# Performance work log

Measured on AMD Instinct MI355X. Metric: run time of the kernel, lower is better.

Reference implementation:

```python
import jax, jax.numpy as jnp
import numpy as np

NUM_ITERATIONS = 5
EPSILON_0 = 1.0
EPS = 1e-20


def setup_inputs() -> dict:
    key = jax.random.key(0)
    k1, k2 = jax.random.split(key)
    B, NIN, NOUT = 8192, 3072, 512
    x = jax.random.uniform(k1, (B, NIN), dtype=jnp.float32)
    w = jax.random.uniform(k2, (NOUT, NIN), dtype=jnp.float32)
    # weights setter normalizes rows to sum to 1
    w = w / w.sum(axis=1, keepdims=True)
    h_initial = jnp.full((NOUT,), 1.0 / NOUT, dtype=jnp.float32)
    return {"x": x, "weights": w, "h_initial": h_initial}


def reference(x, weights, h_initial):
    # x: [B, NIN], weights: [NOUT, NIN], h_initial: [NOUT]
    x = x / (x.sum(axis=1, keepdims=True) + EPS)  # input normalization in forward()
    B = x.shape[0]
    h = jnp.broadcast_to(h_initial[None, :], (B, h_initial.shape[0]))

    def step(h, _):
        # Original: h_w = h[:,:,None]*W[None]; h_w /= h_w.sum(1,keepdim)+eps;
        #           h_w = (h_w * x[:,None,:]).sum(-1)
        # Equivalent without materializing [B, NOUT, NIN]:
        denom = h @ weights                       # [B, NIN] = sum_n h_bn W_nk
        h_w = h * ((x / (denom + EPS)) @ weights.T)  # [B, NOUT]
        h_new = h + EPSILON_0 * h_w               # epsilon_0 > 0 branch
        h_new = h_new / (h_new.sum(axis=1, keepdims=True) + EPS)
        return h_new, None

    h, _ = jax.lax.scan(step, h, None, length=NUM_ITERATIONS)
    return h
```

## Files before the change

### kernel.cpp

```cpp
#include <hip/hip_runtime.h>


#define NIN 3072
#define NOUT 512

using f32x4 = __attribute__((ext_vector_type(4))) float;
using i32x8 = __attribute__((ext_vector_type(8))) int;

union frag32 { i32x8 v; uint4 q[2]; };

#define MFMA128(A, B, C) \
    __builtin_amdgcn_mfma_scale_f32_16x16x128_f8f6f4( \
        (A), (B), (C), 0, 0, 0, (int)0x7f7f7f7f, 0, (int)0x7f7f7f7f)

__device__ __forceinline__ unsigned short f2bf(float f) {
    unsigned int u = __builtin_bit_cast(unsigned int, f);
    return (unsigned short)((u + 0x7fffu + ((u >> 16) & 1u)) >> 16);
}
__device__ __forceinline__ float bf2f(unsigned short s) {
    unsigned int u = ((unsigned int)s) << 16;
    return __builtin_bit_cast(float, u);
}

#define LDS_BARRIER() do {                                   \
    asm volatile("s_waitcnt lgkmcnt(0)" ::: "memory");       \
    __builtin_amdgcn_s_barrier();                            \
    asm volatile("" ::: "memory");                           \
} while (0)

__global__ void prep_all(const float* __restrict__ x,
                         const float* __restrict__ W,
                         const float* __restrict__ h_init,
                         unsigned short* __restrict__ X2,
                         unsigned char* __restrict__ W1,
                         unsigned char* __restrict__ W2,
                         float* __restrict__ d0inv) {
    __shared__ float wsum[4];
    __shared__ float dred[8][32];
    const int bb = blockIdx.x;
    const int t  = threadIdx.x;

    if (bb < 8192) {
        const int b = bb;
        const float4* r4 = reinterpret_cast<const float4*>(x + (size_t)b * NIN);
        float s = 0.f;
        float4 v0 = r4[t], v1 = r4[t + 256], v2 = r4[t + 512];
        s = v0.x + v0.y + v0.z + v0.w + v1.x + v1.y + v1.z + v1.w + v2.x + v2.y + v2.z + v2.w;
        #pragma unroll
        for (int off = 32; off > 0; off >>= 1) s += __shfl_down(s, off, 64);
        int w = t >> 6, l = t & 63;
        if (l == 0) wsum[w] = s;
        __syncthreads();
        float inv = 1.0f / (wsum[0] + wsum[1] + wsum[2] + wsum[3] + 1e-20f);
        unsigned short* orow = X2 + (size_t)b * NIN;
        #pragma unroll
        for (int c = 0; c < 3; ++c) {
            float4 v = (c == 0) ? v0 : (c == 1) ? v1 : v2;
            ushort4 o;
            o.x = f2bf(v.x * inv); o.y = f2bf(v.y * inv);
            o.z = f2bf(v.z * inv); o.w = f2bf(v.w * inv);
            *reinterpret_cast<ushort4*>(orow + (t + c * 256) * 4) = o;
        }
    } else if (bb < 8192 + 384) {
        int tt = (bb - 8192) * 256 + t;
        unsigned int words[8];
        if (tt < 49152) {
            int l = tt & 63, g = tt >> 6;
            int s = g >> 5, rem = g & 31, w = rem >> 2, nt = rem & 3;
            int n = w * 64 + nt * 16 + (l & 15);
            int kbase = s * 128 + ((l >> 4) << 5);
            const float* src = W + (size_t)n * NIN + kbase;
            #pragma unroll
            for (int q = 0; q < 8; ++q) {
                float v0 = src[q * 4 + 0] * 4096.0f, v1 = src[q * 4 + 1] * 4096.0f;
                float v2 = src[q * 4 + 2] * 4096.0f, v3 = src[q * 4 + 3] * 4096.0f;
                int pk = __builtin_amdgcn_cvt_pk_fp8_f32(v0, v1, 0, false);
                pk     = __builtin_amdgcn_cvt_pk_fp8_f32(v2, v3, pk, true);
                words[q] = (unsigned int)pk;
            }
            uint4* dst = reinterpret_cast<uint4*>(W2 + (size_t)tt * 32);
            dst[0] = *reinterpret_cast<uint4*>(&words[0]);
            dst[1] = *reinterpret_cast<uint4*>(&words[4]);
        } else {
            int u = tt - 49152;
            int l = u & 63, g = u >> 6;
            int c = g & 3, sw = g >> 2;
            int w = sw & 7, s = sw >> 3;
            int kout = s * 128 + w * 16 + (l & 15);
            int nbase = c * 128 + ((l >> 4) << 5);
            #pragma unroll
            for (int q = 0; q < 8; ++q) {
                float v0 = W[(size_t)(nbase + q * 4 + 0) * NIN + kout] * 4096.0f;
                float v1 = W[(size_t)(nbase + q * 4 + 1) * NIN + kout] * 4096.0f;
                float v2 = W[(size_t)(nbase + q * 4 + 2) * NIN + kout] * 4096.0f;
                float v3 = W[(size_t)(nbase + q * 4 + 3) * NIN + kout] * 4096.0f;
                int pk = __builtin_amdgcn_cvt_pk_fp8_f32(v0, v1, 0, false);
                pk     = __builtin_amdgcn_cvt_pk_fp8_f32(v2, v3, pk, true);
                words[q] = (unsigned int)pk;
            }
            uint4* dst = reinterpret_cast<uint4*>(W1 + (size_t)u * 32);
            dst[0] = *reinterpret_cast<uint4*>(&words[0]);
            dst[1] = *reinterpret_cast<uint4*>(&words[4]);
        }
    } else {
        int kb = bb - 8576;
        int kid = t & 31, nsub = t >> 5;
        int k = kb * 32 + kid;
        int n0 = nsub * 64;
        float s = 0.f;
        const float* p = W + (size_t)n0 * NIN + k;
        #pragma unroll 8
        for (int n = 0; n < 64; ++n) s += h_init[n0 + n] * p[(size_t)n * NIN];
        dred[nsub][kid] = s;
        __syncthreads();
        if (t < 32) {
            float sm = 1e-20f;
            #pragma unroll
            for (int j = 0; j < 8; ++j) sm += dred[j][t];
            d0inv[kb * 32 + t] = 1.0f / sm;
        }
    }
}

__global__ __launch_bounds__(512, 1) void nnmf_main(
    const unsigned short* __restrict__ X2,
    const unsigned char* __restrict__ W1,
    const unsigned char* __restrict__ W2,
    const float* __restrict__ d0inv,
    const float* __restrict__ h_init,
    float* __restrict__ out)
{
    __shared__ unsigned char  h8_lds[32 * 528];
    __shared__ unsigned short x_lds[32 * 136];
    __shared__ unsigned char  r8_lds[32 * 144];
    __shared__ float red[8][32];

    const int tid = threadIdx.x;
    const int w  = tid >> 6;
    const int l  = tid & 63;
    const int lo = l & 15;
    const int hi = l >> 4;
    const int b0 = blockIdx.x * 32;

    float h_reg[2][4][4];
    #pragma unroll
    for (int nt = 0; nt < 4; ++nt) {
        float hv = h_init[w * 64 + nt * 16 + lo];
        #pragma unroll
        for (int m = 0; m < 2; ++m)
            #pragma unroll
            for (int i = 0; i < 4; ++i)
                h_reg[m][nt][i] = hv;
    }

    const int xrow = tid >> 4, xcc = tid & 15;
    const uint4* xg = reinterpret_cast<const uint4*>(X2 + (size_t)(b0 + xrow) * NIN + xcc * 8);
    unsigned short* xdst = &x_lds[xrow * 136 + xcc * 8];

    const unsigned char* w1base = W1 + (size_t)w * 8192 + (size_t)l * 32;
    const unsigned char* w2base = W2 + ((size_t)(w * 4) * 64 + l) * 32;

    *reinterpret_cast<uint4*>(xdst) = xg[0];
    uint4 xnext = xg[16];
    frag32 w1buf[4];
    __syncthreads();

    const float DSCL = 9.5367431640625e-07f;
    const float TS   = 1.0f / 65536.0f;
    f32x4 tacc[2][4];

    for (int it = 0; it < 5; ++it) {
        #pragma unroll
        for (int m = 0; m < 2; ++m)
            #pragma unroll
            for (int nt = 0; nt < 4; ++nt)
                tacc[m][nt] = (f32x4){0.f, 0.f, 0.f, 0.f};

        for (int s = 0; s < 24; ++s) {
            const int sn  = (s + 1 == 24) ? 0 : s + 1;
            const int sn2 = (s + 2 >= 24) ? (s + 2 - 24) : s + 2;

            uint4 xfut = xg[sn2 * 16];

            frag32 w2v[4];
            {
                const unsigned char* w2p = w2base + (size_t)s * 65536;
                #pragma unroll
                for (int nt = 0; nt < 4; ++nt) {
                    const uint4* p = reinterpret_cast<const uint4*>(w2p + nt * 2048);
                    w2v[nt].q[0] = p[0];
                    w2v[nt].q[1] = p[1];
                }
            }

            f32x4 d0, d1;
            float dv = 0.f;
            if (it == 0) {
                dv = d0inv[s * 128 + w * 16 + lo];
            } else {
                f32x4 a0 = {0,0,0,0}, a1 = {0,0,0,0};
                #pragma unroll
                for (int c = 0; c < 4; ++c) {
                    frag32 ha0, ha1;
                    const uint4* p0 = reinterpret_cast<const uint4*>(
                        &h8_lds[lo * 528 + c * 128 + hi * 32]);
                    const uint4* p1 = reinterpret_cast<const uint4*>(
                        &h8_lds[(16 + lo) * 528 + c * 128 + hi * 32]);
                    ha0.q[0] = p0[0]; ha0.q[1] = p0[1];
                    ha1.q[0] = p1[0]; ha1.q[1] = p1[1];
                    a0 = MFMA128(ha0.v, w1buf[c].v, a0);
                    a1 = MFMA128(ha1.v, w1buf[c].v, a1);
                }
                d0 = a0;
                d1 = a1;
            }

            #pragma unroll
            for (int i = 0; i < 4; ++i) {
                int row0 = hi * 4 + i;
                float x0 = bf2f(x_lds[row0 * 136 + w * 16 + lo]) * 16.0f;
                float x1 = bf2f(x_lds[(16 + row0) * 136 + w * 16 + lo]) * 16.0f;
                float r0, r1;
                if (it == 0) { r0 = x0 * dv; r1 = x1 * dv; }
                else {
                    r0 = x0 * __builtin_amdgcn_rcpf(fmaf(d0[i], DSCL, 1e-20f));
                    r1 = x1 * __builtin_amdgcn_rcpf(fmaf(d1[i], DSCL, 1e-20f));
                }
                int c0 = __builtin_amdgcn_cvt_pk_fp8_f32(r0, r0, 0, false);
                int c1 = __builtin_amdgcn_cvt_pk_fp8_f32(r1, r1, 0, false);
                r8_lds[row0 * 144 + w * 16 + lo] = (unsigned char)(c0 & 0xff);
                r8_lds[(16 + row0) * 144 + w * 16 + lo] = (unsigned char)(c1 & 0xff);
            }
            LDS_BARRIER();

            {
                frag32 ra;
                const uint4* p = reinterpret_cast<const uint4*>(&r8_lds[lo * 144 + hi * 32]);
                ra.q[0] = p[0]; ra.q[1] = p[1];
                #pragma unroll
                for (int nt = 0; nt < 4; ++nt)
                    tacc[0][nt] = MFMA128(ra.v, w2v[nt].v, tacc[0][nt]);
            }

            if (it > 0 || s == 23) {
                const unsigned char* w1p = w1base + (size_t)sn * 65536;
                #pragma unroll
                for (int c = 0; c < 4; ++c) {
                    const uint4* p = reinterpret_cast<const uint4*>(w1p + c * 2048);
                    w1buf[c].q[0] = p[0];
                    w1buf[c].q[1] = p[1];
                }
            }

            {
                frag32 ra;
                const uint4* p = reinterpret_cast<const uint4*>(&r8_lds[(16 + lo) * 144 + hi * 32]);
                ra.q[0] = p[0]; ra.q[1] = p[1];
                #pragma unroll
                for (int nt = 0; nt < 4; ++nt)
                    tacc[1][nt] = MFMA128(ra.v, w2v[nt].v, tacc[1][nt]);
            }

            *reinterpret_cast<uint4*>(xdst) = xnext;
            xnext = xfut;
            LDS_BARRIER();
        }

        float p[2][4];
        #pragma unroll
        for (int m = 0; m < 2; ++m)
            #pragma unroll
            for (int i = 0; i < 4; ++i) p[m][i] = 0.f;

        #pragma unroll
        for (int m = 0; m < 2; ++m)
            #pragma unroll
            for (int nt = 0; nt < 4; ++nt)
                #pragma unroll
                for (int i = 0; i < 4; ++i) {
                    float v = h_reg[m][nt][i] * (1.f + tacc[m][nt][i] * TS);
                    h_reg[m][nt][i] = v;
                    p[m][i] += v;
                }
        #pragma unroll
        for (int mask = 1; mask < 16; mask <<= 1)
            #pragma unroll
            for (int m = 0; m < 2; ++m)
                #pragma unroll
                for (int i = 0; i < 4; ++i)
                    p[m][i] += __shfl_xor(p[m][i], mask, 64);
        if (lo == 0) {
            #pragma unroll
            for (int m = 0; m < 2; ++m)
                #pragma unroll
                for (int i = 0; i < 4; ++i)
                    red[w][m * 16 + hi * 4 + i] = p[m][i];
        }
        __syncthreads();
        float inv[2][4];
        #pragma unroll
        for (int m = 0; m < 2; ++m)
            #pragma unroll
            for (int i = 0; i < 4; ++i) {
                int row = m * 16 + hi * 4 + i;
                float S = 0.f;
                #pragma unroll
                for (int ww = 0; ww < 8; ++ww) S += red[ww][row];
                inv[m][i] = 1.f / (S + 1e-20f);
            }

        if (it < 4) {
            #pragma unroll
            for (int m = 0; m < 2; ++m)
                #pragma unroll
                for (int nt = 0; nt < 4; ++nt)
                    #pragma unroll
                    for (int i = 0; i < 4; ++i) {
                        int row = m * 16 + hi * 4 + i;
                        int col = w * 64 + nt * 16 + lo;
                        float hv = h_reg[m][nt][i] * inv[m][i];
                        h_reg[m][nt][i] = hv;
                        int c = __builtin_amdgcn_cvt_pk_fp8_f32(hv * 256.0f, hv * 256.0f, 0, false);
                        h8_lds[row * 528 + col] = (unsigned char)(c & 0xff);
                    }
            __syncthreads();
        } else {
            #pragma unroll
            for (int m = 0; m < 2; ++m)
                #pragma unroll
                for (int nt = 0; nt < 4; ++nt)
                    #pragma unroll
                    for (int i = 0; i < 4; ++i) {
                        int row = m * 16 + hi * 4 + i;
                        int col = w * 64 + nt * 16 + lo;
                        out[(size_t)(b0 + row) * 512 + col] = h_reg[m][nt][i] * inv[m][i];
                    }
        }
    }
}

extern "C" void kernel_launch(void* const* d_in, const int* in_sizes, int n_in,
                              void* d_out, int out_size, void* d_ws, size_t ws_size,
                              hipStream_t stream) {
    const float* x   = (const float*)d_in[0];
    const float* wgt = (const float*)d_in[1];
    const float* h0  = (const float*)d_in[2];
    float* out = (float*)d_out;

    unsigned short* X2 = (unsigned short*)d_ws;
    unsigned char*  W1 = (unsigned char*)((char*)d_ws + 50331648);
    unsigned char*  W2 = (unsigned char*)((char*)d_ws + 51904512);
    float* d0inv       = (float*)((char*)d_ws + 53477376);

    prep_all<<<8672, 256, 0, stream>>>(x, wgt, h0, X2, W1, W2, d0inv);
    nnmf_main<<<256, 512, 0, stream>>>(X2, W1, W2, d0inv, h0, out);
}
```

Measured before the change: 400.1 us.

## Process two K-steps per barrier pair and keep h in LDS

Restructures the inner k-loop to handle two 128-wide K slices per iteration with double-buffered x and r8 LDS tiles, halving the number of LDS barriers and interleaving W1/W2 loads with MFMA work. h is moved from registers to an fp32 LDS buffer to free VGPRs for the extra W1 fragments, and the x*16 scaling is folded into the prep kernel's normalization. The trade is extra LDS traffic for h and more LDS capacity, against higher register pressure from the doubled buffers.

```diff
diff --git a/kernel.cpp b/kernel.cpp
--- a/kernel.cpp
+++ b/kernel.cpp
@@ -51,7 +51,7 @@
         int w = t >> 6, l = t & 63;
         if (l == 0) wsum[w] = s;
         __syncthreads();
-        float inv = 1.0f / (wsum[0] + wsum[1] + wsum[2] + wsum[3] + 1e-20f);
+        float inv = 16.0f / (wsum[0] + wsum[1] + wsum[2] + wsum[3] + 1e-20f);
         unsigned short* orow = X2 + (size_t)b * NIN;
         #pragma unroll
         for (int c = 0; c < 3; ++c) {
@@ -131,8 +131,9 @@
     float* __restrict__ out)
 {
     __shared__ unsigned char  h8_lds[32 * 528];
-    __shared__ unsigned short x_lds[32 * 136];
-    __shared__ unsigned char  r8_lds[32 * 144];
+    __shared__ float          h32_lds[32 * 516];
+    __shared__ unsigned short x_lds[2][32 * 136];
+    __shared__ unsigned char  r8_lds[2][32 * 144];
     __shared__ float red[8][32];
 
     const int tid = threadIdx.x;
@@ -142,27 +143,22 @@
     const int hi = l >> 4;
     const int b0 = blockIdx.x * 32;
 
-    float h_reg[2][4][4];
-    #pragma unroll
-    for (int nt = 0; nt < 4; ++nt) {
-        float hv = h_init[w * 64 + nt * 16 + lo];
-        #pragma unroll
-        for (int m = 0; m < 2; ++m)
-            #pragma unroll
-            for (int i = 0; i < 4; ++i)
-                h_reg[m][nt][i] = hv;
+    for (int idx = tid; idx < 32 * 512; idx += 512) {
+        int r = idx >> 9, c = idx & 511;
+        h32_lds[r * 516 + c] = h_init[c];
     }
 
     const int xrow = tid >> 4, xcc = tid & 15;
     const uint4* xg = reinterpret_cast<const uint4*>(X2 + (size_t)(b0 + xrow) * NIN + xcc * 8);
-    unsigned short* xdst = &x_lds[xrow * 136 + xcc * 8];
+    const int xoff = xrow * 136 + xcc * 8;
 
     const unsigned char* w1base = W1 + (size_t)w * 8192 + (size_t)l * 32;
     const unsigned char* w2base = W2 + ((size_t)(w * 4) * 64 + l) * 32;
 
-    *reinterpret_cast<uint4*>(xdst) = xg[0];
-    uint4 xnext = xg[16];
-    frag32 w1buf[4];
+    *reinterpret_cast<uint4*>(&x_lds[0][xoff]) = xg[0];
+    *reinterpret_cast<uint4*>(&x_lds[1][xoff]) = xg[16];
+    uint4 xnA = xg[32], xnB = xg[48];
+    frag32 w1A[4], w1B[4];
     __syncthreads();
 
     const float DSCL = 9.5367431640625e-07f;
@@ -176,96 +172,156 @@
             for (int nt = 0; nt < 4; ++nt)
                 tacc[m][nt] = (f32x4){0.f, 0.f, 0.f, 0.f};
 
-        for (int s = 0; s < 24; ++s) {
-            const int sn  = (s + 1 == 24) ? 0 : s + 1;
-            const int sn2 = (s + 2 >= 24) ? (s + 2 - 24) : s + 2;
-
-            uint4 xfut = xg[sn2 * 16];
-
-            frag32 w2v[4];
+        for (int t = 0; t < 12; ++t) {
+            const int s = 2 * t;
+
+            float dvA = 0.f, dvB = 0.f;
+            if (it == 0) {
+                dvA = d0inv[s * 128 + w * 16 + lo];
+                dvB = d0inv[(s + 1) * 128 + w * 16 + lo];
+            }
+
+            f32x4 dA0 = {0,0,0,0}, dB0 = {0,0,0,0};
+            if (it != 0) {
+                #pragma unroll
+                for (int c = 0; c < 4; ++c) {
+                    frag32 ha;
+                    const uint4* p = reinterpret_cast<const uint4*>(
+                        &h8_lds[lo * 528 + c * 128 + hi * 32]);
+                    ha.q[0] = p[0]; ha.q[1] = p[1];
+                    dA0 = MFMA128(ha.v, w1A[c].v, dA0);
+                    dB0 = MFMA128(ha.v, w1B[c].v, dB0);
+                }
+            }
+            #pragma unroll
+            for (int i = 0; i < 4; ++i) {
+                int row0 = hi * 4 + i;
+                float xA = bf2f(x_lds[0][row0 * 136 + w * 16 + lo]);
+                float xB = bf2f(x_lds[1][row0 * 136 + w * 16 + lo]);
+                float rA, rB;
+                if (it == 0) { rA = xA * dvA; rB = xB * dvB; }
+                else {
+                    rA = xA * __builtin_amdgcn_rcpf(fmaf(dA0[i], DSCL, 1e-20f));
+                    rB = xB * __builtin_amdgcn_rcpf(fmaf(dB0[i], DSCL, 1e-20f));
+                }
+                int cA = __builtin_amdgcn_cvt_pk_fp8_f32(rA, rA, 0, false);
+                int cB = __builtin_amdgcn_cvt_pk_fp8_f32(rB, rB, 0, false);
+                r8_lds[0][row0 * 144 + w * 16 + lo] = (unsigned char)(cA & 0xff);
+                r8_lds[1][row0 * 144 + w * 16 + lo] = (unsigned char)(cB & 0xff);
+            }
+
+            f32x4 dA1 = {0,0,0,0}, dB1 = {0,0,0,0};
+            if (it != 0) {
+                #pragma unroll
+                for (int c = 0; c < 4; ++c) {
+                    frag32 ha;
+                    const uint4* p = reinterpret_cast<const uint4*>(
+                        &h8_lds[(16 + lo) * 528 + c * 128 + hi * 32]);
+                    ha.q[0] = p[0]; ha.q[1] = p[1];
+                    dA1 = MFMA128(ha.v, w1A[c].v, dA1);
+                    dB1 = MFMA128(ha.v, w1B[c].v, dB1);
+                }
+            }
+
+            frag32 w2vA[4];
             {
                 const unsigned char* w2p = w2base + (size_t)s * 65536;
                 #pragma unroll
                 for (int nt = 0; nt < 4; ++nt) {
                     const uint4* p = reinterpret_cast<const uint4*>(w2p + nt * 2048);
-                    w2v[nt].q[0] = p[0];
-                    w2v[nt].q[1] = p[1];
-                }
-            }
-
-            f32x4 d0, d1;
-            float dv = 0.f;
-            if (it == 0) {
-                dv = d0inv[s * 128 + w * 16 + lo];
-            } else {
-                f32x4 a0 = {0,0,0,0}, a1 = {0,0,0,0};
-                #pragma unroll
-                for (int c = 0; c < 4; ++c) {
-                    frag32 ha0, ha1;
-                    const uint4* p0 = reinterpret_cast<const uint4*>(
-                        &h8_lds[lo * 528 + c * 128 + hi * 32]);
-                    const uint4* p1 = reinterpret_cast<const uint4*>(
-                        &h8_lds[(16 + lo) * 528 + c * 128 + hi * 32]);
-                    ha0.q[0] = p0[0]; ha0.q[1] = p0[1];
-                    ha1.q[0] = p1[0]; ha1.q[1] = p1[1];
-                    a0 = MFMA128(ha0.v, w1buf[c].v, a0);
-                    a1 = MFMA128(ha1.v, w1buf[c].v, a1);
-                }
-                d0 = a0;
-                d1 = a1;
+                    w2vA[nt].q[0] = p[0];
+                    w2vA[nt].q[1] = p[1];
+                }
             }
 
             #pragma unroll
             for (int i = 0; i < 4; ++i) {
-                int row0 = hi * 4 + i;
-                float x0 = bf2f(x_lds[row0 * 136 + w * 16 + lo]) * 16.0f;
-                float x1 = bf2f(x_lds[(16 + row0) * 136 + w * 16 + lo]) * 16.0f;
-                float r0, r1;
-                if (it == 0) { r0 = x0 * dv; r1 = x1 * dv; }
+                int row1 = 16 + hi * 4 + i;
+                float xA = bf2f(x_lds[0][row1 * 136 + w * 16 + lo]);
+                float xB = bf2f(x_lds[1][row1 * 136 + w * 16 + lo]);
+                float rA, rB;
+                if (it == 0) { rA = xA * dvA; rB = xB * dvB; }
                 else {
-                    r0 = x0 * __builtin_amdgcn_rcpf(fmaf(d0[i], DSCL, 1e-20f));
-                    r1 = x1 * __builtin_amdgcn_rcpf(fmaf(d1[i], DSCL, 1e-20f));
-                }
-                int c0 = __builtin_amdgcn_cvt_pk_fp8_f32(r0, r0, 0, false);
-                int c1 = __builtin_amdgcn_cvt_pk_fp8_f32(r1, r1, 0, false);
-                r8_lds[row0 * 144 + w * 16 + lo] = (unsigned char)(c0 & 0xff);
-                r8_lds[(16 + row0) * 144 + w * 16 + lo] = (unsigned char)(c1 & 0xff);
+                    rA = xA * __builtin_amdgcn_rcpf(fmaf(dA1[i], DSCL, 1e-20f));
+                    rB = xB * __builtin_amdgcn_rcpf(fmaf(dB1[i], DSCL, 1e-20f));
+                }
+                int cA = __builtin_amdgcn_cvt_pk_fp8_f32(rA, rA, 0, false);
+                int cB = __builtin_amdgcn_cvt_pk_fp8_f32(rB, rB, 0, false);
+                r8_lds[0][row1 * 144 + w * 16 + lo] = (unsigned char)(cA & 0xff);
+                r8_lds[1][row1 * 144 + w * 16 + lo] = (unsigned char)(cB & 0xff);
             }
             LDS_BARRIER();
 
             {
-                frag32 ra;
-                const uint4* p = reinterpret_cast<const uint4*>(&r8_lds[lo * 144 + hi * 32]);
-                ra.q[0] = p[0]; ra.q[1] = p[1];
-                #pragma unroll
-                for (int nt = 0; nt < 4; ++nt)
-                    tacc[0][nt] = MFMA128(ra.v, w2v[nt].v, tacc[0][nt]);
-            }
-
-            if (it > 0 || s == 23) {
-                const unsigned char* w1p = w1base + (size_t)sn * 65536;
+                frag32 ra0, ra1;
+                const uint4* p0 = reinterpret_cast<const uint4*>(&r8_lds[0][lo * 144 + hi * 32]);
+                const uint4* p1 = reinterpret_cast<const uint4*>(&r8_lds[0][(16 + lo) * 144 + hi * 32]);
+                ra0.q[0] = p0[0]; ra0.q[1] = p0[1];
+                ra1.q[0] = p1[0]; ra1.q[1] = p1[1];
+                #pragma unroll
+                for (int nt = 0; nt < 4; ++nt) {
+                    tacc[0][nt] = MFMA128(ra0.v, w2vA[nt].v, tacc[0][nt]);
+                    tacc[1][nt] = MFMA128(ra1.v, w2vA[nt].v, tacc[1][nt]);
+                }
+            }
+
+            frag32 w2vB[4];
+            {
+                const unsigned char* w2p = w2base + (size_t)(s + 1) * 65536;
+                #pragma unroll
+                for (int nt = 0; nt < 4; ++nt) {
+                    const uint4* p = reinterpret_cast<const uint4*>(w2p + nt * 2048);
+                    w2vB[nt].q[0] = p[0];
+                    w2vB[nt].q[1] = p[1];
+                }
+            }
+            if (it > 0 || t == 11) {
+                int sw = (t == 11) ? 0 : s + 2;
+                const unsigned char* w1p = w1base + (size_t)sw * 65536;
                 #pragma unroll
                 for (int c = 0; c < 4; ++c) {
                     const uint4* p = reinterpret_cast<const uint4*>(w1p + c * 2048);
-                    w1buf[c].q[0] = p[0];
-                    w1buf[c].q[1] = p[1];
+                    w1A[c].q[0] = p[0];
+                    w1A[c].q[1] = p[1];
                 }
             }
 
             {
-                frag32 ra;
-                const uint4* p = reinterpret_cast<const uint4*>(&r8_lds[(16 + lo) * 144 + hi * 32]);
-                ra.q[0] = p[0]; ra.q[1] = p[1];
-                #pragma unroll
-                for (int nt = 0; nt < 4; ++nt)
-                    tacc[1][nt] = MFMA128(ra.v, w2v[nt].v, tacc[1][nt]);
-            }
-
-            *reinterpret_cast<uint4*>(xdst) = xnext;
-            xnext = xfut;
+                frag32 ra0, ra1;
+                const uint4* p0 = reinterpret_cast<const uint4*>(&r8_lds[1][lo * 144 + hi * 32]);
+                const uint4* p1 = reinterpret_cast<const uint4*>(&r8_lds[1][(16 + lo) * 144 + hi * 32]);
+                ra0.q[0] = p0[0]; ra0.q[1] = p0[1];
+                ra1.q[0] = p1[0]; ra1.q[1] = p1[1];
+                #pragma unroll
+                for (int nt = 0; nt < 4; ++nt) {
+                    tacc[0][nt] = MFMA128(ra0.v, w2vB[nt].v, tacc[0][nt]);
+                    tacc[1][nt] = MFMA128(ra1.v, w2vB[nt].v, tacc[1][nt]);
+                }
+            }
+
+            if (it > 0 || t == 11) {
+                int sw = (t == 11) ? 1 : s + 3;
+                const unsigned char* w1p = w1base + (size_t)sw * 65536;
+                #pragma unroll
+                for (int c = 0; c < 4; ++c) {
+                    const uint4* p = reinterpret_cast<const uint4*>(w1p + c * 2048);
+                    w1B[c].q[0] = p[0];
+                    w1B[c].q[1] = p[1];
+                }
+            }
+
+            *reinterpret_cast<uint4*>(&x_lds[0][xoff]) = xnA;
+            *reinterpret_cast<uint4*>(&x_lds[1][xoff]) = xnB;
+            {
+                int fA = s + 4; if (fA >= 24) fA -= 24;
+                int fB = s + 5; if (fB >= 24) fB -= 24;
+                xnA = xg[(size_t)fA * 16];
+                xnB = xg[(size_t)fB * 16];
+            }
             LDS_BARRIER();
         }
 
+        float hv_[2][4][4];
         float p[2][4];
         #pragma unroll
         for (int m = 0; m < 2; ++m)
@@ -278,8 +334,11 @@
             for (int nt = 0; nt < 4; ++nt)
                 #pragma unroll
                 for (int i = 0; i < 4; ++i) {
-                    float v = h_reg[m][nt][i] * (1.f + tacc[m][nt][i] * TS);
-                    h_reg[m][nt][i] = v;
+                    int row = m * 16 + hi * 4 + i;
+                    int col = w * 64 + nt * 16 + lo;
+                    float hv = h32_lds[row * 516 + col];
+                    float v = hv * (1.f + tacc[m][nt][i] * TS);
+                    hv_[m][nt][i] = v;
                     p[m][i] += v;
                 }
         #pragma unroll
@@ -318,8 +377,8 @@
                     for (int i = 0; i < 4; ++i) {
                         int row = m * 16 + hi * 4 + i;
                         int col = w * 64 + nt * 16 + lo;
-                        float hv = h_reg[m][nt][i] * inv[m][i];
-                        h_reg[m][nt][i] = hv;
+                        float hv = hv_[m][nt][i] * inv[m][i];
+                        h32_lds[row * 516 + col] = hv;
                         int c = __builtin_amdgcn_cvt_pk_fp8_f32(hv * 256.0f, hv * 256.0f, 0, false);
                         h8_lds[row * 528 + col] = (unsigned char)(c & 0xff);
                     }
@@ -333,7 +392,7 @@
                     for (int i = 0; i < 4; ++i) {
                         int row = m * 16 + hi * 4 + i;
                         int col = w * 64 + nt * 16 + lo;
-                        out[(size_t)(b0 + row) * 512 + col] = h_reg[m][nt][i] * inv[m][i];
+                        out[(size_t)(b0 + row) * 512 + col] = hv_[m][nt][i] * inv[m][i];
                     }
         }
     }
```

Result: slower. 413.4 us (+3.3%).

## Stage W2 tiles via global_load_lds into swizzled LDS, split MFMA accumulators

Applied to the files above, without the earlier changes.

The W2 fragments are now copied straight from global memory into a 64KB LDS staging buffer with global_load_lds, instead of being loaded into registers, and then read back from LDS. The prep kernel stores W2 in an XOR-swizzled layout to avoid LDS bank conflicts on that read-back. The denominator MFMA chain is split into two independent accumulators to shorten dependency latency. The x prescale by 16 moves into the normalization kernel. The large LDS buffer and an explicit vmcnt(0) wait before the barrier trade occupancy headroom and some overlap for lower register pressure.

```diff
diff --git a/kernel.cpp b/kernel.cpp
--- a/kernel.cpp
+++ b/kernel.cpp
@@ -51,7 +51,7 @@
         int w = t >> 6, l = t & 63;
         if (l == 0) wsum[w] = s;
         __syncthreads();
-        float inv = 1.0f / (wsum[0] + wsum[1] + wsum[2] + wsum[3] + 1e-20f);
+        float inv = 16.0f / (wsum[0] + wsum[1] + wsum[2] + wsum[3] + 1e-20f);
         unsigned short* orow = X2 + (size_t)b * NIN;
         #pragma unroll
         for (int c = 0; c < 3; ++c) {
@@ -78,9 +78,12 @@
                 pk     = __builtin_amdgcn_cvt_pk_fp8_f32(v2, v3, pk, true);
                 words[q] = (unsigned int)pk;
             }
-            uint4* dst = reinterpret_cast<uint4*>(W2 + (size_t)tt * 32);
-            dst[0] = *reinterpret_cast<uint4*>(&words[0]);
-            dst[1] = *reinterpret_cast<uint4*>(&words[4]);
+            unsigned int b0 = (unsigned int)tt * 32;
+            unsigned int sw = ((b0 >> 7) & 7u) << 4;
+            *reinterpret_cast<uint4*>(W2 + (b0 ^ sw)) =
+                *reinterpret_cast<uint4*>(&words[0]);
+            *reinterpret_cast<uint4*>(W2 + ((b0 | 16u) ^ sw)) =
+                *reinterpret_cast<uint4*>(&words[4]);
         } else {
             int u = tt - 49152;
             int l = u & 63, g = u >> 6;
@@ -130,6 +133,7 @@
     const float* __restrict__ h_init,
     float* __restrict__ out)
 {
+    __shared__ unsigned char  w2stage[65536];
     __shared__ unsigned char  h8_lds[32 * 528];
     __shared__ unsigned short x_lds[32 * 136];
     __shared__ unsigned char  r8_lds[32 * 144];
@@ -158,7 +162,9 @@
     unsigned short* xdst = &x_lds[xrow * 136 + xcc * 8];
 
     const unsigned char* w1base = W1 + (size_t)w * 8192 + (size_t)l * 32;
-    const unsigned char* w2base = W2 + ((size_t)(w * 4) * 64 + l) * 32;
+    const unsigned char* w2dma  = W2 + (size_t)w * 8192 + (size_t)l * 16;
+    const int slz = (l * 32) ^ (((l >> 2) & 7) << 4);
+    const unsigned char* wsbase = w2stage + w * 8192;
 
     *reinterpret_cast<uint4*>(xdst) = xg[0];
     uint4 xnext = xg[16];
@@ -180,46 +186,54 @@
             const int sn  = (s + 1 == 24) ? 0 : s + 1;
             const int sn2 = (s + 2 >= 24) ? (s + 2 - 24) : s + 2;
 
+            {
+                const unsigned char* gsrc = w2dma + (size_t)s * 65536;
+                #pragma unroll
+                for (int j = 0; j < 8; ++j) {
+                    __builtin_amdgcn_global_load_lds(
+                        (const __attribute__((address_space(1))) unsigned int*)(gsrc + j * 1024),
+                        (__attribute__((address_space(3))) unsigned int*)(w2stage + w * 8192 + j * 1024),
+                        16, 0, 0);
+                }
+            }
+
             uint4 xfut = xg[sn2 * 16];
-
-            frag32 w2v[4];
-            {
-                const unsigned char* w2p = w2base + (size_t)s * 65536;
-                #pragma unroll
-                for (int nt = 0; nt < 4; ++nt) {
-                    const uint4* p = reinterpret_cast<const uint4*>(w2p + nt * 2048);
-                    w2v[nt].q[0] = p[0];
-                    w2v[nt].q[1] = p[1];
-                }
-            }
 
             f32x4 d0, d1;
             float dv = 0.f;
             if (it == 0) {
                 dv = d0inv[s * 128 + w * 16 + lo];
             } else {
-                f32x4 a0 = {0,0,0,0}, a1 = {0,0,0,0};
-                #pragma unroll
-                for (int c = 0; c < 4; ++c) {
-                    frag32 ha0, ha1;
-                    const uint4* p0 = reinterpret_cast<const uint4*>(
+                f32x4 a0a = {0,0,0,0}, a0b = {0,0,0,0}, a1a = {0,0,0,0}, a1b = {0,0,0,0};
+                #pragma unroll
+                for (int c = 0; c < 4; c += 2) {
+                    frag32 h0a, h1a, h0b, h1b;
+                    const uint4* p0a = reinterpret_cast<const uint4*>(
                         &h8_lds[lo * 528 + c * 128 + hi * 32]);
-                    const uint4* p1 = reinterpret_cast<const uint4*>(
+                    const uint4* p1a = reinterpret_cast<const uint4*>(
                         &h8_lds[(16 + lo) * 528 + c * 128 + hi * 32]);
-                    ha0.q[0] = p0[0]; ha0.q[1] = p0[1];
-                    ha1.q[0] = p1[0]; ha1.q[1] = p1[1];
-                    a0 = MFMA128(ha0.v, w1buf[c].v, a0);
-                    a1 = MFMA128(ha1.v, w1buf[c].v, a1);
-                }
-                d0 = a0;
-                d1 = a1;
+                    const uint4* p0b = reinterpret_cast<const uint4*>(
+                        &h8_lds[lo * 528 + (c + 1) * 128 + hi * 32]);
+                    const uint4* p1b = reinterpret_cast<const uint4*>(
+                        &h8_lds[(16 + lo) * 528 + (c + 1) * 128 + hi * 32]);
+                    h0a.q[0] = p0a[0]; h0a.q[1] = p0a[1];
+                    h1a.q[0] = p1a[0]; h1a.q[1] = p1a[1];
+                    h0b.q[0] = p0b[0]; h0b.q[1] = p0b[1];
+                    h1b.q[0] = p1b[0]; h1b.q[1] = p1b[1];
+                    a0a = MFMA128(h0a.v, w1buf[c].v,     a0a);
+                    a1a = MFMA128(h1a.v, w1buf[c].v,     a1a);
+                    a0b = MFMA128(h0b.v, w1buf[c + 1].v, a0b);
+                    a1b = MFMA128(h1b.v, w1buf[c + 1].v, a1b);
+                }
+                d0 = a0a + a0b;
+                d1 = a1a + a1b;
             }
 
             #pragma unroll
             for (int i = 0; i < 4; ++i) {
                 int row0 = hi * 4 + i;
-                float x0 = bf2f(x_lds[row0 * 136 + w * 16 + lo]) * 16.0f;
-                float x1 = bf2f(x_lds[(16 + row0) * 136 + w * 16 + lo]) * 16.0f;
+                float x0 = bf2f(x_lds[row0 * 136 + w * 16 + lo]);
+                float x1 = bf2f(x_lds[(16 + row0) * 136 + w * 16 + lo]);
                 float r0, r1;
                 if (it == 0) { r0 = x0 * dv; r1 = x1 * dv; }
                 else {
@@ -231,15 +245,25 @@
                 r8_lds[row0 * 144 + w * 16 + lo] = (unsigned char)(c0 & 0xff);
                 r8_lds[(16 + row0) * 144 + w * 16 + lo] = (unsigned char)(c1 & 0xff);
             }
+
+            asm volatile("s_waitcnt vmcnt(0)" ::: "memory");
+            __builtin_amdgcn_sched_barrier(0);
             LDS_BARRIER();
 
+            frag32 ra0, ra1;
             {
-                frag32 ra;
-                const uint4* p = reinterpret_cast<const uint4*>(&r8_lds[lo * 144 + hi * 32]);
-                ra.q[0] = p[0]; ra.q[1] = p[1];
-                #pragma unroll
-                for (int nt = 0; nt < 4; ++nt)
-                    tacc[0][nt] = MFMA128(ra.v, w2v[nt].v, tacc[0][nt]);
+                const uint4* p0 = reinterpret_cast<const uint4*>(&r8_lds[lo * 144 + hi * 32]);
+                const uint4* p1 = reinterpret_cast<const uint4*>(&r8_lds[(16 + lo) * 144 + hi * 32]);
+                ra0.q[0] = p0[0]; ra0.q[1] = p0[1];
+                ra1.q[0] = p1[0]; ra1.q[1] = p1[1];
+            }
+            #pragma unroll
+            for (int nt = 0; nt < 2; ++nt) {
+                frag32 wf;
+                wf.q[0] = *reinterpret_cast<const uint4*>(wsbase + nt * 2048 + slz);
+                wf.q[1] = *reinterpret_cast<const uint4*>(wsbase + nt * 2048 + (slz ^ 16));
+                tacc[0][nt] = MFMA128(ra0.v, wf.v, tacc[0][nt]);
+                tacc[1][nt] = MFMA128(ra1.v, wf.v, tacc[1][nt]);
             }
 
             if (it > 0 || s == 23) {
@@ -252,13 +276,13 @@
                 }
             }
 
-            {
-                frag32 ra;
-                const uint4* p = reinterpret_cast<const uint4*>(&r8_lds[(16 + lo) * 144 + hi * 32]);
-                ra.q[0] = p[0]; ra.q[1] = p[1];
-                #pragma unroll
-                for (int nt = 0; nt < 4; ++nt)
-                    tacc[1][nt] = MFMA128(ra.v, w2v[nt].v, tacc[1][nt]);
+            #pragma unroll
+            for (int nt = 2; nt < 4; ++nt) {
+                frag32 wf;
+                wf.q[0] = *reinterpret_cast<const uint4*>(wsbase + nt * 2048 + slz);
+                wf.q[1] = *reinterpret_cast<const uint4*>(wsbase + nt * 2048 + (slz ^ 16));
+                tacc[0][nt] = MFMA128(ra0.v, wf.v, tacc[0][nt]);
+                tacc[1][nt] = MFMA128(ra1.v, wf.v, tacc[1][nt]);
             }
 
             *reinterpret_cast<uint4*>(xdst) = xnext;
```

Result: slower. 447.6 us (+11.9%).

## Keep fp32 h state in LDS, interleave MFMAs, fold x scale into prep

Applied to the files above, without the earlier changes.

The per-thread fp32 h state (32 floats) moves out of registers into a padded shared-memory array, cutting register pressure in the main loop. The second matmul now loads both row-halves of the fp8 r fragment first and interleaves their MFMAs across the W1 prefetch. The global load of a future x tile is issued later in each step, which shortens how long its registers stay live. The ×16 scale on x moves into the normalization kernel. In exchange the kernel uses about 66KB more LDS and adds LDS reads and writes of h in every iteration epilogue.

```diff
diff --git a/kernel.cpp b/kernel.cpp
--- a/kernel.cpp
+++ b/kernel.cpp
@@ -51,7 +51,7 @@
         int w = t >> 6, l = t & 63;
         if (l == 0) wsum[w] = s;
         __syncthreads();
-        float inv = 1.0f / (wsum[0] + wsum[1] + wsum[2] + wsum[3] + 1e-20f);
+        float inv = 16.0f / (wsum[0] + wsum[1] + wsum[2] + wsum[3] + 1e-20f);
         unsigned short* orow = X2 + (size_t)b * NIN;
         #pragma unroll
         for (int c = 0; c < 3; ++c) {
@@ -131,6 +131,7 @@
     float* __restrict__ out)
 {
     __shared__ unsigned char  h8_lds[32 * 528];
+    __shared__ float          h32_lds[32 * 516];
     __shared__ unsigned short x_lds[32 * 136];
     __shared__ unsigned char  r8_lds[32 * 144];
     __shared__ float red[8][32];
@@ -142,15 +143,9 @@
     const int hi = l >> 4;
     const int b0 = blockIdx.x * 32;
 
-    float h_reg[2][4][4];
-    #pragma unroll
-    for (int nt = 0; nt < 4; ++nt) {
-        float hv = h_init[w * 64 + nt * 16 + lo];
-        #pragma unroll
-        for (int m = 0; m < 2; ++m)
-            #pragma unroll
-            for (int i = 0; i < 4; ++i)
-                h_reg[m][nt][i] = hv;
+    for (int idx = tid; idx < 32 * 512; idx += 512) {
+        int r = idx >> 9, c = idx & 511;
+        h32_lds[r * 516 + c] = h_init[c];
     }
 
     const int xrow = tid >> 4, xcc = tid & 15;
@@ -158,7 +153,7 @@
     unsigned short* xdst = &x_lds[xrow * 136 + xcc * 8];
 
     const unsigned char* w1base = W1 + (size_t)w * 8192 + (size_t)l * 32;
-    const unsigned char* w2base = W2 + ((size_t)(w * 4) * 64 + l) * 32;
+    const unsigned char* w2base = W2 + (size_t)w * 8192 + (size_t)l * 32;
 
     *reinterpret_cast<uint4*>(xdst) = xg[0];
     uint4 xnext = xg[16];
@@ -180,8 +175,6 @@
             const int sn  = (s + 1 == 24) ? 0 : s + 1;
             const int sn2 = (s + 2 >= 24) ? (s + 2 - 24) : s + 2;
 
-            uint4 xfut = xg[sn2 * 16];
-
             frag32 w2v[4];
             {
                 const unsigned char* w2p = w2base + (size_t)s * 65536;
@@ -193,12 +186,11 @@
                 }
             }
 
-            f32x4 d0, d1;
+            f32x4 d0 = {0,0,0,0}, d1 = {0,0,0,0};
             float dv = 0.f;
             if (it == 0) {
                 dv = d0inv[s * 128 + w * 16 + lo];
             } else {
-                f32x4 a0 = {0,0,0,0}, a1 = {0,0,0,0};
                 #pragma unroll
                 for (int c = 0; c < 4; ++c) {
                     frag32 ha0, ha1;
@@ -208,18 +200,16 @@
                         &h8_lds[(16 + lo) * 528 + c * 128 + hi * 32]);
                     ha0.q[0] = p0[0]; ha0.q[1] = p0[1];
                     ha1.q[0] = p1[0]; ha1.q[1] = p1[1];
-                    a0 = MFMA128(ha0.v, w1buf[c].v, a0);
-                    a1 = MFMA128(ha1.v, w1buf[c].v, a1);
-                }
-                d0 = a0;
-                d1 = a1;
+                    d0 = MFMA128(ha0.v, w1buf[c].v, d0);
+                    d1 = MFMA128(ha1.v, w1buf[c].v, d1);
+                }
             }
 
             #pragma unroll
             for (int i = 0; i < 4; ++i) {
                 int row0 = hi * 4 + i;
-                float x0 = bf2f(x_lds[row0 * 136 + w * 16 + lo]) * 16.0f;
-                float x1 = bf2f(x_lds[(16 + row0) * 136 + w * 16 + lo]) * 16.0f;
+                float x0 = bf2f(x_lds[row0 * 136 + w * 16 + lo]);
+                float x1 = bf2f(x_lds[(16 + row0) * 136 + w * 16 + lo]);
                 float r0, r1;
                 if (it == 0) { r0 = x0 * dv; r1 = x1 * dv; }
                 else {
@@ -233,13 +223,17 @@
             }
             LDS_BARRIER();
 
+            frag32 ra0, ra1;
             {
-                frag32 ra;
-                const uint4* p = reinterpret_cast<const uint4*>(&r8_lds[lo * 144 + hi * 32]);
-                ra.q[0] = p[0]; ra.q[1] = p[1];
-                #pragma unroll
-                for (int nt = 0; nt < 4; ++nt)
-                    tacc[0][nt] = MFMA128(ra.v, w2v[nt].v, tacc[0][nt]);
+                const uint4* p0 = reinterpret_cast<const uint4*>(&r8_lds[lo * 144 + hi * 32]);
+                const uint4* p1 = reinterpret_cast<const uint4*>(&r8_lds[(16 + lo) * 144 + hi * 32]);
+                ra0.q[0] = p0[0]; ra0.q[1] = p0[1];
+                ra1.q[0] = p1[0]; ra1.q[1] = p1[1];
+            }
+            #pragma unroll
+            for (int nt = 0; nt < 2; ++nt) {
+                tacc[0][nt] = MFMA128(ra0.v, w2v[nt].v, tacc[0][nt]);
+                tacc[1][nt] = MFMA128(ra1.v, w2v[nt].v, tacc[1][nt]);
             }
 
             if (it > 0 || s == 23) {
@@ -252,20 +246,18 @@
                 }
             }
 
-            {
-                frag32 ra;
-                const uint4* p = reinterpret_cast<const uint4*>(&r8_lds[(16 + lo) * 144 + hi * 32]);
-                ra.q[0] = p[0]; ra.q[1] = p[1];
-                #pragma unroll
-                for (int nt = 0; nt < 4; ++nt)
-                    tacc[1][nt] = MFMA128(ra.v, w2v[nt].v, tacc[1][nt]);
+            #pragma unroll
+            for (int nt = 2; nt < 4; ++nt) {
+                tacc[0][nt] = MFMA128(ra0.v, w2v[nt].v, tacc[0][nt]);
+                tacc[1][nt] = MFMA128(ra1.v, w2v[nt].v, tacc[1][nt]);
             }
 
             *reinterpret_cast<uint4*>(xdst) = xnext;
-            xnext = xfut;
+            xnext = xg[(size_t)sn2 * 16];
             LDS_BARRIER();
         }
 
+        float hv_[2][4][4];
         float p[2][4];
         #pragma unroll
         for (int m = 0; m < 2; ++m)
@@ -278,8 +270,11 @@
             for (int nt = 0; nt < 4; ++nt)
                 #pragma unroll
                 for (int i = 0; i < 4; ++i) {
-                    float v = h_reg[m][nt][i] * (1.f + tacc[m][nt][i] * TS);
-                    h_reg[m][nt][i] = v;
+                    int row = m * 16 + hi * 4 + i;
+                    int col = w * 64 + nt * 16 + lo;
+                    float hv = h32_lds[row * 516 + col];
+                    float v = hv * (1.f + tacc[m][nt][i] * TS);
+                    hv_[m][nt][i] = v;
                     p[m][i] += v;
                 }
         #pragma unroll
@@ -318,8 +313,8 @@
                     for (int i = 0; i < 4; ++i) {
                         int row = m * 16 + hi * 4 + i;
                         int col = w * 64 + nt * 16 + lo;
-                        float hv = h_reg[m][nt][i] * inv[m][i];
-                        h_reg[m][nt][i] = hv;
+                        float hv = hv_[m][nt][i] * inv[m][i];
+                        h32_lds[row * 516 + col] = hv;
                         int c = __builtin_amdgcn_cvt_pk_fp8_f32(hv * 256.0f, hv * 256.0f, 0, false);
                         h8_lds[row * 528 + col] = (unsigned char)(c & 0xff);
                     }
@@ -333,7 +328,7 @@
                     for (int i = 0; i < 4; ++i) {
                         int row = m * 16 + hi * 4 + i;
                         int col = w * 64 + nt * 16 + lo;
-                        out[(size_t)(b0 + row) * 512 + col] = h_reg[m][nt][i] * inv[m][i];
+                        out[(size_t)(b0 + row) * 512 + col] = hv_[m][nt][i] * inv[m][i];
                     }
         }
     }
```

Measured after the change: 391.2 us. 1.02x faster.
